# Performance work log

Measured on AMD Instinct MI355X. Metric: run time of the kernel, lower is better.

The kernel has to match this reference:

```python
import jax, jax.numpy as jnp
import numpy as np

NUM_HEADS = 16
HEAD_DIM = 80
DIM = NUM_HEADS * HEAD_DIM
SEQ = 2048
SCALE = HEAD_DIM ** -0.5


def rotate_half(x):
    x1, x2 = jnp.split(x, 2, axis=-1)
    return jnp.concatenate((-x2, x1), axis=-1)


def setup_inputs() -> dict:
    key = jax.random.key(0)
    ks = jax.random.split(key, 8)
    hidden_states = jax.random.normal(ks[0], (SEQ, DIM), dtype=jnp.float32)
    cu_seqlens = jnp.array([0, SEQ], dtype=jnp.int32)  # unused by the math
    # rotary embeddings for head_dim
    inv_freq = 1.0 / (10000.0 ** (jnp.arange(0, HEAD_DIM // 2, dtype=jnp.float32) / (HEAD_DIM // 2)))
    freqs = jnp.outer(jnp.arange(SEQ, dtype=jnp.float32), inv_freq)  # [S, hd/2]
    emb = jnp.concatenate((freqs, freqs), axis=-1)  # [S, hd]
    cos = jnp.cos(emb)
    sin = jnp.sin(emb)
    w_qkv = jax.random.normal(ks[1], (3 * DIM, DIM), dtype=jnp.float32) * (DIM ** -0.5)
    b_qkv = jax.random.normal(ks[2], (3 * DIM,), dtype=jnp.float32) * 0.02
    w_proj = jax.random.normal(ks[3], (DIM, DIM), dtype=jnp.float32) * (DIM ** -0.5)
    b_proj = jax.random.normal(ks[4], (DIM,), dtype=jnp.float32) * 0.02
    return {"hidden_states": hidden_states, "cu_seqlens": cu_seqlens, "cos": cos,
            "sin": sin, "w_qkv": w_qkv, "b_qkv": b_qkv, "w_proj": w_proj, "b_proj": b_proj}


def reference(hidden_states, cu_seqlens, cos, sin, w_qkv, b_qkv, w_proj, b_proj):
    S = hidden_states.shape[0]
    qkv = hidden_states @ w_qkv.T + b_qkv  # [S, 3*D]
    qkv = qkv.reshape(S, 3, NUM_HEADS, HEAD_DIM)
    q, k, v = qkv[:, 0], qkv[:, 1], qkv[:, 2]  # each [S, H, hd]
    c = cos[:, None, :]  # [S, 1, hd]
    s = sin[:, None, :]
    q = q * c + rotate_half(q) * s
    k = k * c + rotate_half(k) * s
    # SDPA, non-causal: [H, S, S]
    scores = jnp.einsum('shd,thd->hst', q, k) * SCALE
    attn = jax.nn.softmax(scores, axis=-1)
    out = jnp.einsum('hst,thd->shd', attn, v).reshape(S, DIM)
    return out @ w_proj.T + b_proj
```

## Files before the change

kernel.cpp:

```cpp
#include <hip/hip_runtime.h>


#define SEQLEN   2048
#define DIMM     1280
#define NHEADS   16
#define HD       80
#define QKV_N    3840
#define NSPLIT   4
#define KVSPAN   (SEQLEN / NSPLIT)
#define QSCALE_LOG2E 0.16130083587064776f

#define KSTRIDE  88
#define VFSTRIDE 24

#define EXP2F(x) __builtin_amdgcn_exp2f(x)

#define GLD16(gptr, lptr)                                                      \
    __builtin_amdgcn_global_load_lds(                                          \
        (const __attribute__((address_space(1))) void*)(gptr),                 \
        (__attribute__((address_space(3))) void*)(lptr), 16, 0, 0)

typedef float f32x4 __attribute__((ext_vector_type(4)));
typedef _Float16 half8 __attribute__((ext_vector_type(8)));
typedef _Float16 half4 __attribute__((ext_vector_type(4)));
typedef _Float16 half2v __attribute__((ext_vector_type(2)));

static __device__ __forceinline__ f32x4 mfma_16x16x32(half8 a, half8 b, f32x4 c) {
    return __builtin_amdgcn_mfma_f32_16x16x32_f16(a, b, c, 0, 0, 0);
}
static __device__ __forceinline__ f32x4 mfma_16x16x16(half4 a, half4 b, f32x4 c) {
    return __builtin_amdgcn_mfma_f32_16x16x16f16(a, b, c, 0, 0, 0);
}
static __device__ __forceinline__ half4 lo4(half8 v) {
    return __builtin_shufflevector(v, v, 0, 1, 2, 3);
}
static __device__ __forceinline__ half4 hi4(half8 v) {
    return __builtin_shufflevector(v, v, 4, 5, 6, 7);
}

__global__ __launch_bounds__(256)
void cast_all(const float* __restrict__ hs, const float* __restrict__ wq,
              const float* __restrict__ wp, _Float16* __restrict__ dhs,
              _Float16* __restrict__ dwq, _Float16* __restrict__ dwp) {
    const int n1 = SEQLEN * DIMM / 4, n2 = QKV_N * DIMM / 4, n3 = DIMM * DIMM / 4;
    int i = blockIdx.x * 256 + threadIdx.x;
    const float4* src; half4* dst; int j;
    if (i < n1)           { src = (const float4*)hs; dst = (half4*)dhs; j = i; }
    else if (i < n1 + n2) { src = (const float4*)wq; dst = (half4*)dwq; j = i - n1; }
    else if (i < n1 + n2 + n3) { src = (const float4*)wp; dst = (half4*)dwp; j = i - n1 - n2; }
    else return;
    const float4 v = src[j];
    half4 h;
    h.x = (_Float16)v.x; h.y = (_Float16)v.y;
    h.z = (_Float16)v.z; h.w = (_Float16)v.w;
    dst[j] = h;
}

template<bool OUT_F16>
__global__ __launch_bounds__(512, 4)
void gemm_bt128(const _Float16* __restrict__ A, const _Float16* __restrict__ B,
                const float* __restrict__ bias, void* __restrict__ Cout,
                int M, int N, int K) {
    __shared__ __align__(16) _Float16 As[2][128 * 32];
    __shared__ __align__(16) _Float16 Bs[2][128 * 32];
    const int tid  = threadIdx.x;
    const int lane = tid & 63;
    const int wave = tid >> 6;
    const int l15  = lane & 15;
    const int quad = lane >> 4;
    const int wm   = wave & 3;
    const int wn   = wave >> 2;
    const long bm = blockIdx.x, bn = blockIdx.y;

    const _Float16* Ag = A + bm * 128 * (long)K;
    const _Float16* Bg = B + bn * 128 * (long)K;

    const int srow = lane >> 2;
    const int scol = (lane & 3) * 8;
    f32x4 acc[2][4] = {};

    for (int k0 = 0; k0 < K; k0 += 64) {
        __syncthreads();
#pragma unroll
        for (int p = 0; p < 2; p++) {
            const int kp = k0 + p * 32;
            const long r = 16 * wave + srow;
            GLD16(Ag + r * K + kp + scol, &As[p][512 * wave + lane * 8]);
            GLD16(Bg + r * K + kp + scol, &Bs[p][512 * wave + lane * 8]);
        }
        __syncthreads();
#pragma unroll
        for (int p = 0; p < 2; p++) {
            half8 af[2], bf[4];
#pragma unroll
            for (int t = 0; t < 2; t++)
                af[t] = *(const half8*)&As[p][(wm * 32 + t * 16 + l15) * 32 + quad * 8];
#pragma unroll
            for (int t = 0; t < 4; t++)
                bf[t] = *(const half8*)&Bs[p][(wn * 64 + t * 16 + l15) * 32 + quad * 8];
#pragma unroll
            for (int mt = 0; mt < 2; mt++)
#pragma unroll
                for (int nt = 0; nt < 4; nt++)
                    acc[mt][nt] = mfma_16x16x32(af[mt], bf[nt], acc[mt][nt]);
        }
    }

    float bv[4];
#pragma unroll
    for (int nt = 0; nt < 4; nt++)
        bv[nt] = bias[bn * 128 + wn * 64 + nt * 16 + l15];

#pragma unroll
    for (int mt = 0; mt < 2; mt++) {
#pragma unroll
        for (int r = 0; r < 4; r++) {
            const long row = bm * 128 + wm * 32 + mt * 16 + quad * 4 + r;
#pragma unroll
            for (int nt = 0; nt < 4; nt++) {
                const long col = bn * 128 + wn * 64 + nt * 16 + l15;
                const float v = acc[mt][nt][r] + bv[nt];
                if (OUT_F16) ((_Float16*)Cout)[row * (long)N + col] = (_Float16)v;
                else         ((float*)Cout)[row * (long)N + col] = v;
            }
        }
    }
}

template<bool OUT_F16>
__global__ __launch_bounds__(256, 4)
void gemm_bt64(const _Float16* __restrict__ A, const _Float16* __restrict__ B,
               const float* __restrict__ bias, void* __restrict__ Cout,
               int M, int N, int K) {
    __shared__ __align__(16) _Float16 As[2][64 * 32];
    __shared__ __align__(16) _Float16 Bs[2][128 * 32];
    const int tid  = threadIdx.x;
    const int lane = tid & 63;
    const int wave = tid >> 6;
    const int l15  = lane & 15;
    const int quad = lane >> 4;
    const int wm   = wave & 1;
    const int wn   = wave >> 1;
    const long bm = blockIdx.x, bn = blockIdx.y;

    const _Float16* Ag = A + bm * 64 * (long)K;
    const _Float16* Bg = B + bn * 128 * (long)K;

    const int srow = lane >> 2;
    const int scol = (lane & 3) * 8;
    f32x4 acc[2][4] = {};

    for (int k0 = 0; k0 < K; k0 += 64) {
        __syncthreads();
#pragma unroll
        for (int p = 0; p < 2; p++) {
            const int kp = k0 + p * 32;
            const long arow = 16 * wave + srow;
            GLD16(Ag + arow * K + kp + scol, &As[p][512 * wave + lane * 8]);
#pragma unroll
            for (int cc = 0; cc < 2; cc++) {
                const int c = wave + cc * 4;
                const long brow = 16 * c + srow;
                GLD16(Bg + brow * K + kp + scol, &Bs[p][512 * c + lane * 8]);
            }
        }
        __syncthreads();
#pragma unroll
        for (int p = 0; p < 2; p++) {
            half8 af[2], bf[4];
#pragma unroll
            for (int t = 0; t < 2; t++)
                af[t] = *(const half8*)&As[p][(wm * 32 + t * 16 + l15) * 32 + quad * 8];
#pragma unroll
            for (int t = 0; t < 4; t++)
                bf[t] = *(const half8*)&Bs[p][(wn * 64 + t * 16 + l15) * 32 + quad * 8];
#pragma unroll
            for (int mt = 0; mt < 2; mt++)
#pragma unroll
                for (int nt = 0; nt < 4; nt++)
                    acc[mt][nt] = mfma_16x16x32(af[mt], bf[nt], acc[mt][nt]);
        }
    }

    float bv[4];
#pragma unroll
    for (int nt = 0; nt < 4; nt++)
        bv[nt] = bias[bn * 128 + wn * 64 + nt * 16 + l15];

#pragma unroll
    for (int mt = 0; mt < 2; mt++) {
#pragma unroll
        for (int r = 0; r < 4; r++) {
            const long row = bm * 64 + wm * 32 + mt * 16 + quad * 4 + r;
#pragma unroll
            for (int nt = 0; nt < 4; nt++) {
                const long col = bn * 128 + wn * 64 + nt * 16 + l15;
                const float v = acc[mt][nt][r] + bv[nt];
                if (OUT_F16) ((_Float16*)Cout)[row * (long)N + col] = (_Float16)v;
                else         ((float*)Cout)[row * (long)N + col] = v;
            }
        }
    }
}

__global__ __launch_bounds__(256)
void rope_repack_t(const _Float16* __restrict__ qkv,
                   const float* __restrict__ cosb,
                   const float* __restrict__ sinb,
                   _Float16* __restrict__ Qh,
                   _Float16* __restrict__ Kh,
                   _Float16* __restrict__ Vt) {
    const int s0 = blockIdx.x * 64;
    const int h  = blockIdx.y;
    __shared__ __align__(16) _Float16 Ts[64 * 88];
    const int tid = threadIdx.x;

    for (int i = tid; i < 640; i += 256) {
        const int r = i / 10, c = (i - r * 10) * 8;
        *(half8*)&Ts[r * 88 + c] =
            *(const half8*)&qkv[(long)(s0 + r) * QKV_N + 2 * DIMM + h * HD + c];
    }

    for (int i = tid; i < 320; i += 256) {
        const int r = i / 5, d = (i - r * 5) * 8;
        const _Float16* row = qkv + (long)(s0 + r) * QKV_N + h * HD;
        const half8 q0 = *(const half8*)&row[d];
        const half8 q1 = *(const half8*)&row[d + 40];
        const half8 k0 = *(const half8*)&row[DIMM + d];
        const half8 k1 = *(const half8*)&row[DIMM + d + 40];
        const float4 cA = *(const float4*)&cosb[(s0 + r) * HD + d];
        const float4 cB = *(const float4*)&cosb[(s0 + r) * HD + d + 4];
        const float4 sA = *(const float4*)&sinb[(s0 + r) * HD + d];
        const float4 sB = *(const float4*)&sinb[(s0 + r) * HD + d + 4];
        half8 qo0, qo1, ko0, ko1;
#pragma unroll
        for (int j = 0; j < 8; j++) {
            const float cj = (j < 4) ? cA[j] : cB[j - 4];
            const float sj = (j < 4) ? sA[j] : sB[j - 4];
            qo0[j] = (_Float16)(((float)q0[j] * cj - (float)q1[j] * sj) * QSCALE_LOG2E);
            qo1[j] = (_Float16)(((float)q1[j] * cj + (float)q0[j] * sj) * QSCALE_LOG2E);
            ko0[j] = (_Float16)((float)k0[j] * cj - (float)k1[j] * sj);
            ko1[j] = (_Float16)((float)k1[j] * cj + (float)k0[j] * sj);
        }
        const long o = ((long)h * SEQLEN + s0 + r) * HD;
        *(half8*)&Qh[o + d]      = qo0;
        *(half8*)&Qh[o + d + 40] = qo1;
        *(half8*)&Kh[o + d]      = ko0;
        *(half8*)&Kh[o + d + 40] = ko1;
    }
    __syncthreads();
    for (int i = tid; i < 640; i += 256) {
        const int d = i >> 3, sc = (i & 7) * 8;
        half8 v;
#pragma unroll
        for (int j = 0; j < 8; j++) v[j] = Ts[(sc + j) * 88 + d];
        *(half8*)&Vt[((long)h * HD + d) * SEQLEN + s0 + sc] = v;
    }
}

__global__ __launch_bounds__(512, 4)
void attn_kernel(const _Float16* __restrict__ Qh, const _Float16* __restrict__ Kh,
                 const _Float16* __restrict__ Vt,
                 _Float16* __restrict__ Ohat0, _Float16* __restrict__ Ohat1,
                 float* __restrict__ Lpart) {
    const int s0 = blockIdx.x * 256;
    const int h  = blockIdx.y;
    const int z  = blockIdx.z;
    __shared__ __align__(16) _Float16 Ks[64 * KSTRIDE];
    __shared__ __align__(16) _Float16 VF[5 * 64 * VFSTRIDE];

    const int tid  = threadIdx.x;
    const int lane = tid & 63;
    const int wave = tid >> 6;
    const int l15  = lane & 15;
    const int quad = lane >> 4;

    const int zBeg = z * KVSPAN, zEnd = zBeg + KVSPAN;

    const _Float16* Qg0 = Qh + ((long)h * SEQLEN + s0 + wave * 32 + l15) * HD;
    const _Float16* Qg1 = Qg0 + 16 * (long)HD;
    const half8 qA0 = *(const half8*)&Qg0[quad * 8];
    const half8 qA1 = *(const half8*)&Qg0[32 + quad * 8];
    const half4 qA2 = *(const half4*)&Qg0[64 + quad * 4];
    const half8 qB0 = *(const half8*)&Qg1[quad * 8];
    const half8 qB1 = *(const half8*)&Qg1[32 + quad * 8];
    const half4 qB2 = *(const half4*)&Qg1[64 + quad * 4];

    int offA, dsA, offB, dsB0, dsB1 = 0, offC = 0, dsC0 = 0, dsC1 = 0;
    {
        const int rA = tid / 10, cA = (tid - rA * 10) * 8;
        offA = rA * HD + cA;
        dsA  = rA * KSTRIDE + cA;
        if (tid < 128) {
            const int cB = tid + 512;
            const int rB = cB / 10, ccB = (cB - rB * 10) * 8;
            offB = rB * HD + ccB;
            dsB0 = rB * KSTRIDE + ccB;
        } else {
            const int v = tid - 128, d = v >> 3, c8 = (v & 7) * 8;
            offB = d * SEQLEN + c8;
            const int nt = d >> 4, ld = d & 15, ct = c8 >> 4, qb = (c8 & 15) >> 2;
            dsB0 = (nt * 64 + qb * 16 + ld) * VFSTRIDE + ct * 4;
            dsB1 = (nt * 64 + (qb + 1) * 16 + ld) * VFSTRIDE + ct * 4;
        }
        if (tid < 256) {
            const int v = tid + 384, d = v >> 3, c8 = (v & 7) * 8;
            offC = d * SEQLEN + c8;
            const int nt = d >> 4, ld = d & 15, ct = c8 >> 4, qb = (c8 & 15) >> 2;
            dsC0 = (nt * 64 + qb * 16 + ld) * VFSTRIDE + ct * 4;
            dsC1 = (nt * 64 + (qb + 1) * 16 + ld) * VFSTRIDE + ct * 4;
        }
    }
    const _Float16* KzBase = Kh + ((long)h * SEQLEN + zBeg) * HD;
    const _Float16* VzBase = Vt + (long)h * HD * SEQLEN + zBeg;

    half8 sga, sgb, sgc = (half8)(_Float16)0.f;
    sga = *(const half8*)(KzBase + offA);
    if (tid < 128) sgb = *(const half8*)(KzBase + offB);
    else           sgb = *(const half8*)(VzBase + offB);
    if (tid < 256) sgc = *(const half8*)(VzBase + offC);

    f32x4 oaccA[5] = {}, oaccB[5] = {};
    float laA0 = 0.f, laA1 = 0.f, laB0 = 0.f, laB1 = 0.f;
    const half2v ones2 = {(_Float16)1.f, (_Float16)1.f};

    for (int t0 = zBeg; t0 < zEnd; t0 += 64) {
        __syncthreads();
        *(half8*)&Ks[dsA] = sga;
        if (tid < 128) { *(half8*)&Ks[dsB0] = sgb; }
        else {
            *(half4*)&VF[dsB0] = lo4(sgb);
            *(half4*)&VF[dsB1] = hi4(sgb);
        }
        if (tid < 256) {
            *(half4*)&VF[dsC0] = lo4(sgc);
            *(half4*)&VF[dsC1] = hi4(sgc);
        }
        __syncthreads();

        if (t0 + 64 < zEnd) {
            const _Float16* KzT = KzBase + (long)(t0 + 64 - zBeg) * HD;
            const _Float16* VzT = VzBase + (t0 + 64 - zBeg);
            sga = *(const half8*)(KzT + offA);
            if (tid < 128) sgb = *(const half8*)(KzT + offB);
            else           sgb = *(const half8*)(VzT + offB);
            if (tid < 256) sgc = *(const half8*)(VzT + offC);
        }

        f32x4 saA[4] = {}, saB[4] = {};
        __builtin_amdgcn_s_setprio(1);
#pragma unroll
        for (int ct = 0; ct < 4; ct++) {
            const int kb = (ct * 16 + l15) * KSTRIDE;
            const half8 kf0 = *(const half8*)&Ks[kb + quad * 8];
            const half8 kf1 = *(const half8*)&Ks[kb + 32 + quad * 8];
            const half4 kf2 = *(const half4*)&Ks[kb + 64 + quad * 4];
            saA[ct] = mfma_16x16x32(kf0, qA0, saA[ct]);
            saB[ct] = mfma_16x16x32(kf0, qB0, saB[ct]);
            saA[ct] = mfma_16x16x32(kf1, qA1, saA[ct]);
            saB[ct] = mfma_16x16x32(kf1, qB1, saB[ct]);
            saA[ct] = mfma_16x16x16(kf2, qA2, saA[ct]);
            saB[ct] = mfma_16x16x16(kf2, qB2, saB[ct]);
        }
        __builtin_amdgcn_s_setprio(0);

        half4 pbA[4], pbB[4];
#pragma unroll
        for (int ct = 0; ct < 4; ct++) {
            {
                const float e0 = EXP2F(saA[ct][0]);
                const float e1 = EXP2F(saA[ct][1]);
                const float e2 = EXP2F(saA[ct][2]);
                const float e3 = EXP2F(saA[ct][3]);
                const half2v p01 = __builtin_bit_cast(half2v, __builtin_amdgcn_cvt_pkrtz(e0, e1));
                const half2v p23 = __builtin_bit_cast(half2v, __builtin_amdgcn_cvt_pkrtz(e2, e3));
                laA0 = __builtin_amdgcn_fdot2(p01, ones2, laA0, false);
                laA1 = __builtin_amdgcn_fdot2(p23, ones2, laA1, false);
                pbA[ct] = __builtin_shufflevector(p01, p23, 0, 1, 2, 3);
            }
            {
                const float e0 = EXP2F(saB[ct][0]);
                const float e1 = EXP2F(saB[ct][1]);
                const float e2 = EXP2F(saB[ct][2]);
                const float e3 = EXP2F(saB[ct][3]);
                const half2v p01 = __builtin_bit_cast(half2v, __builtin_amdgcn_cvt_pkrtz(e0, e1));
                const half2v p23 = __builtin_bit_cast(half2v, __builtin_amdgcn_cvt_pkrtz(e2, e3));
                laB0 = __builtin_amdgcn_fdot2(p01, ones2, laB0, false);
                laB1 = __builtin_amdgcn_fdot2(p23, ones2, laB1, false);
                pbB[ct] = __builtin_shufflevector(p01, p23, 0, 1, 2, 3);
            }
        }

        __builtin_amdgcn_s_setprio(1);
#pragma unroll
        for (int nt = 0; nt < 5; nt++) {
            const half8 va = *(const half8*)&VF[(nt * 64 + lane) * VFSTRIDE];
            const half8 vb = *(const half8*)&VF[(nt * 64 + lane) * VFSTRIDE + 8];
            oaccA[nt] = mfma_16x16x16(lo4(va), pbA[0], oaccA[nt]);
            oaccB[nt] = mfma_16x16x16(lo4(va), pbB[0], oaccB[nt]);
            oaccA[nt] = mfma_16x16x16(hi4(va), pbA[1], oaccA[nt]);
            oaccB[nt] = mfma_16x16x16(hi4(va), pbB[1], oaccB[nt]);
            oaccA[nt] = mfma_16x16x16(lo4(vb), pbA[2], oaccA[nt]);
            oaccB[nt] = mfma_16x16x16(lo4(vb), pbB[2], oaccB[nt]);
            oaccA[nt] = mfma_16x16x16(hi4(vb), pbA[3], oaccA[nt]);
            oaccB[nt] = mfma_16x16x16(hi4(vb), pbB[3], oaccB[nt]);
        }
        __builtin_amdgcn_s_setprio(0);
    }

    float lA = laA0 + laA1, lB = laB0 + laB1;
    lA += __shfl_xor(lA, 16); lA += __shfl_xor(lA, 32);
    lB += __shfl_xor(lB, 16); lB += __shfl_xor(lB, 32);
    const float invA = 1.0f / lA, invB = 1.0f / lB;

    _Float16* Oz = (z < 2) ? Ohat0 : Ohat1;
    const long obase = ((long)(z & 1) * NHEADS + h) * SEQLEN;
    const long lbase = ((long)z * NHEADS + h) * SEQLEN;
    const long rowA = s0 + wave * 32 + l15;
    const long rowB = rowA + 16;
#pragma unroll
    for (int nt = 0; nt < 5; nt++) {
        half4 oA, oB;
#pragma unroll
        for (int r = 0; r < 4; r++) {
            oA[r] = (_Float16)(oaccA[nt][r] * invA);
            oB[r] = (_Float16)(oaccB[nt][r] * invB);
        }
        *(half4*)&Oz[(obase + rowA) * HD + nt * 16 + quad * 4] = oA;
        *(half4*)&Oz[(obase + rowB) * HD + nt * 16 + quad * 4] = oB;
    }
    if (quad == 0) {
        Lpart[lbase + rowA] = lA;
        Lpart[lbase + rowB] = lB;
    }
}

__global__ __launch_bounds__(256)
void attn_combine(const _Float16* __restrict__ Ohat0,
                  const _Float16* __restrict__ Ohat1,
                  const float* __restrict__ Lp,
                  _Float16* __restrict__ attnb) {
    const int i = blockIdx.x * 256 + threadIdx.x;
    if (i >= SEQLEN * DIMM / 8) return;
    const int flat = i * 8;
    const int s = flat / DIMM;
    const int rem = flat - s * DIMM;
    const int h = rem / HD;
    const int d = rem - h * HD;
    float l[NSPLIT], lsum = 0.f;
#pragma unroll
    for (int zi = 0; zi < NSPLIT; zi++) {
        l[zi] = Lp[((long)zi * NHEADS + h) * SEQLEN + s];
        lsum += l[zi];
    }
    const float invl = 1.0f / lsum;
    float acc[8] = {};
#pragma unroll
    for (int zi = 0; zi < NSPLIT; zi++) {
        const _Float16* Oz = (zi < 2) ? Ohat0 : Ohat1;
        const long obase = ((long)(zi & 1) * NHEADS + h) * SEQLEN;
        const half8 o = *(const half8*)&Oz[(obase + s) * HD + d];
        const float w = l[zi] * invl;
#pragma unroll
        for (int j = 0; j < 8; j++) acc[j] += (float)o[j] * w;
    }
    half8 o;
#pragma unroll
    for (int j = 0; j < 8; j++) o[j] = (_Float16)acc[j];
    *(half8*)&attnb[(long)s * DIMM + rem] = o;
}

extern "C" void kernel_launch(void* const* d_in, const int* in_sizes, int n_in,
                              void* d_out, int out_size, void* d_ws, size_t ws_size,
                              hipStream_t stream) {
    const float* hs     = (const float*)d_in[0];
    const float* cosb   = (const float*)d_in[2];
    const float* sinb   = (const float*)d_in[3];
    const float* w_qkv  = (const float*)d_in[4];
    const float* b_qkv  = (const float*)d_in[5];
    const float* w_proj = (const float*)d_in[6];
    const float* b_proj = (const float*)d_in[7];
    float* out = (float*)d_out;

    _Float16* hsb    = (_Float16*)d_ws;
    _Float16* wqkvb  = hsb    + (long)SEQLEN * DIMM;
    _Float16* wprojb = wqkvb  + (long)QKV_N * DIMM;
    _Float16* qkv    = wprojb + (long)DIMM * DIMM;
    _Float16* Qh     = qkv    + (long)SEQLEN * QKV_N;
    _Float16* Kh     = Qh     + (long)NHEADS * SEQLEN * HD;
    _Float16* Vtb    = Kh     + (long)NHEADS * SEQLEN * HD;
    _Float16* attnb  = Vtb    + (long)NHEADS * HD * SEQLEN;

    _Float16* Ohat0  = (_Float16*)d_ws;
    float*    LpartB = (float*)(Ohat0 + (long)2 * NHEADS * SEQLEN * HD);
    _Float16* Ohat1  = qkv;

    {
        const int ntot = (SEQLEN * DIMM + QKV_N * DIMM + DIMM * DIMM) / 4;
        cast_all<<<(ntot + 255) / 256, 256, 0, stream>>>(
            hs, w_qkv, w_proj, hsb, wqkvb, wprojb);
    }

    gemm_bt128<true><<<dim3(SEQLEN / 128, QKV_N / 128), 512, 0, stream>>>(
        hsb, wqkvb, b_qkv, qkv, SEQLEN, QKV_N, DIMM);

    rope_repack_t<<<dim3(SEQLEN / 64, NHEADS), 256, 0, stream>>>(
        qkv, cosb, sinb, Qh, Kh, Vtb);

    attn_kernel<<<dim3(SEQLEN / 256, NHEADS, NSPLIT), 512, 0, stream>>>(
        Qh, Kh, Vtb, Ohat0, Ohat1, LpartB);

    attn_combine<<<(SEQLEN * DIMM / 8 + 255) / 256, 256, 0, stream>>>(
        Ohat0, Ohat1, LpartB, attnb);

    gemm_bt64<false><<<dim3(SEQLEN / 64, DIMM / 128), 256, 0, stream>>>(
        attnb, wprojb, b_proj, out, SEQLEN, DIMM, DIMM);
}
```

Measured before the change: 188.1 us.

## Double-buffer LDS tiles in both GEMM kernels to overlap loads with MFMA

Both GEMM kernels now keep two LDS buffers and issue async global-to-LDS loads for the next K-slice before running the MFMAs on the current slice, with one barrier per iteration instead of two. The aim is to hide global load latency behind matrix compute. LDS use per block doubles, and the bt64 launch bound drops to 3 blocks per SM, which may reduce occupancy. There is no explicit vmcnt wait before the barrier, so correctness relies on the compiler inserting waits for the LDS-direct loads.

```diff
diff --git a/kernel.cpp b/kernel.cpp
--- a/kernel.cpp
+++ b/kernel.cpp
@@ -61,8 +61,8 @@
 void gemm_bt128(const _Float16* __restrict__ A, const _Float16* __restrict__ B,
                 const float* __restrict__ bias, void* __restrict__ Cout,
                 int M, int N, int K) {
-    __shared__ __align__(16) _Float16 As[2][128 * 32];
-    __shared__ __align__(16) _Float16 Bs[2][128 * 32];
+    __shared__ __align__(16) _Float16 As[2][2][128 * 32];
+    __shared__ __align__(16) _Float16 Bs[2][2][128 * 32];
     const int tid  = threadIdx.x;
     const int lane = tid & 63;
     const int wave = tid >> 6;
@@ -77,33 +77,41 @@
 
     const int srow = lane >> 2;
     const int scol = (lane & 3) * 8;
+    const long r   = 16 * wave + srow;
     f32x4 acc[2][4] = {};
 
-    for (int k0 = 0; k0 < K; k0 += 64) {
-        __syncthreads();
+    auto stage = [&](int b, int k0) {
 #pragma unroll
         for (int p = 0; p < 2; p++) {
             const int kp = k0 + p * 32;
-            const long r = 16 * wave + srow;
-            GLD16(Ag + r * K + kp + scol, &As[p][512 * wave + lane * 8]);
-            GLD16(Bg + r * K + kp + scol, &Bs[p][512 * wave + lane * 8]);
-        }
-        __syncthreads();
+            GLD16(Ag + r * K + kp + scol, &As[b][p][512 * wave + lane * 8]);
+            GLD16(Bg + r * K + kp + scol, &Bs[b][p][512 * wave + lane * 8]);
+        }
+    };
+
+    stage(0, 0);
+    __syncthreads();
+
+    int cb = 0;
+    for (int k0 = 0; k0 < K; k0 += 64) {
+        if (k0 + 64 < K) stage(cb ^ 1, k0 + 64);
 #pragma unroll
         for (int p = 0; p < 2; p++) {
             half8 af[2], bf[4];
 #pragma unroll
             for (int t = 0; t < 2; t++)
-                af[t] = *(const half8*)&As[p][(wm * 32 + t * 16 + l15) * 32 + quad * 8];
+                af[t] = *(const half8*)&As[cb][p][(wm * 32 + t * 16 + l15) * 32 + quad * 8];
 #pragma unroll
             for (int t = 0; t < 4; t++)
-                bf[t] = *(const half8*)&Bs[p][(wn * 64 + t * 16 + l15) * 32 + quad * 8];
+                bf[t] = *(const half8*)&Bs[cb][p][(wn * 64 + t * 16 + l15) * 32 + quad * 8];
 #pragma unroll
             for (int mt = 0; mt < 2; mt++)
 #pragma unroll
                 for (int nt = 0; nt < 4; nt++)
                     acc[mt][nt] = mfma_16x16x32(af[mt], bf[nt], acc[mt][nt]);
         }
+        __syncthreads();
+        cb ^= 1;
     }
 
     float bv[4];
@@ -114,12 +122,12 @@
 #pragma unroll
     for (int mt = 0; mt < 2; mt++) {
 #pragma unroll
-        for (int r = 0; r < 4; r++) {
-            const long row = bm * 128 + wm * 32 + mt * 16 + quad * 4 + r;
+        for (int rr = 0; rr < 4; rr++) {
+            const long row = bm * 128 + wm * 32 + mt * 16 + quad * 4 + rr;
 #pragma unroll
             for (int nt = 0; nt < 4; nt++) {
                 const long col = bn * 128 + wn * 64 + nt * 16 + l15;
-                const float v = acc[mt][nt][r] + bv[nt];
+                const float v = acc[mt][nt][rr] + bv[nt];
                 if (OUT_F16) ((_Float16*)Cout)[row * (long)N + col] = (_Float16)v;
                 else         ((float*)Cout)[row * (long)N + col] = v;
             }
@@ -128,12 +136,12 @@
 }
 
 template<bool OUT_F16>
-__global__ __launch_bounds__(256, 4)
+__global__ __launch_bounds__(256, 3)
 void gemm_bt64(const _Float16* __restrict__ A, const _Float16* __restrict__ B,
                const float* __restrict__ bias, void* __restrict__ Cout,
                int M, int N, int K) {
-    __shared__ __align__(16) _Float16 As[2][64 * 32];
-    __shared__ __align__(16) _Float16 Bs[2][128 * 32];
+    __shared__ __align__(16) _Float16 As[2][2][64 * 32];
+    __shared__ __align__(16) _Float16 Bs[2][2][128 * 32];
     const int tid  = threadIdx.x;
     const int lane = tid & 63;
     const int wave = tid >> 6;
@@ -150,36 +158,44 @@
     const int scol = (lane & 3) * 8;
     f32x4 acc[2][4] = {};
 
-    for (int k0 = 0; k0 < K; k0 += 64) {
-        __syncthreads();
+    auto stage = [&](int b, int k0) {
 #pragma unroll
         for (int p = 0; p < 2; p++) {
             const int kp = k0 + p * 32;
             const long arow = 16 * wave + srow;
-            GLD16(Ag + arow * K + kp + scol, &As[p][512 * wave + lane * 8]);
+            GLD16(Ag + arow * K + kp + scol, &As[b][p][512 * wave + lane * 8]);
 #pragma unroll
             for (int cc = 0; cc < 2; cc++) {
                 const int c = wave + cc * 4;
                 const long brow = 16 * c + srow;
-                GLD16(Bg + brow * K + kp + scol, &Bs[p][512 * c + lane * 8]);
+                GLD16(Bg + brow * K + kp + scol, &Bs[b][p][512 * c + lane * 8]);
             }
         }
-        __syncthreads();
+    };
+
+    stage(0, 0);
+    __syncthreads();
+
+    int cb = 0;
+    for (int k0 = 0; k0 < K; k0 += 64) {
+        if (k0 + 64 < K) stage(cb ^ 1, k0 + 64);
 #pragma unroll
         for (int p = 0; p < 2; p++) {
             half8 af[2], bf[4];
 #pragma unroll
             for (int t = 0; t < 2; t++)
-                af[t] = *(const half8*)&As[p][(wm * 32 + t * 16 + l15) * 32 + quad * 8];
+                af[t] = *(const half8*)&As[cb][p][(wm * 32 + t * 16 + l15) * 32 + quad * 8];
 #pragma unroll
             for (int t = 0; t < 4; t++)
-                bf[t] = *(const half8*)&Bs[p][(wn * 64 + t * 16 + l15) * 32 + quad * 8];
+                bf[t] = *(const half8*)&Bs[cb][p][(wn * 64 + t * 16 + l15) * 32 + quad * 8];
 #pragma unroll
             for (int mt = 0; mt < 2; mt++)
 #pragma unroll
                 for (int nt = 0; nt < 4; nt++)
                     acc[mt][nt] = mfma_16x16x32(af[mt], bf[nt], acc[mt][nt]);
         }
+        __syncthreads();
+        cb ^= 1;
     }
 
     float bv[4];
@@ -190,12 +206,12 @@
 #pragma unroll
     for (int mt = 0; mt < 2; mt++) {
 #pragma unroll
-        for (int r = 0; r < 4; r++) {
-            const long row = bm * 64 + wm * 32 + mt * 16 + quad * 4 + r;
+        for (int rr = 0; rr < 4; rr++) {
+            const long row = bm * 64 + wm * 32 + mt * 16 + quad * 4 + rr;
 #pragma unroll
             for (int nt = 0; nt < 4; nt++) {
                 const long col = bn * 128 + wn * 64 + nt * 16 + l15;
-                const float v = acc[mt][nt][r] + bv[nt];
+                const float v = acc[mt][nt][rr] + bv[nt];
                 if (OUT_F16) ((_Float16*)Cout)[row * (long)N + col] = (_Float16)v;
                 else         ((float*)Cout)[row * (long)N + col] = v;
             }
```

Result: no change. 188.8 us (+0.4%).

## Stage 128-key K/V tiles per barrier pair and drop register prefetch

Applied to the files above, without the earlier changes.

The attention kernel now stages 128 keys of K and V into shared memory per iteration instead of 64, halving the number of barrier pairs per KV span. Each tile is processed as two 64-key halves with the same MFMA and exp code. The register-held prefetch of the next tile is removed, so global loads are issued at the top of each iteration and their latency is exposed before the store to LDS. Shared memory per block roughly doubles, which may lower occupancy. Separately, the gemm_bt64 launch bound is relaxed from 4 to 2 blocks per CU, giving the compiler more registers.

```diff
diff --git a/kernel.cpp b/kernel.cpp
--- a/kernel.cpp
+++ b/kernel.cpp
@@ -8,10 +8,12 @@
 #define QKV_N    3840
 #define NSPLIT   4
 #define KVSPAN   (SEQLEN / NSPLIT)
+#define KVBLK    128
 #define QSCALE_LOG2E 0.16130083587064776f
 
 #define KSTRIDE  88
 #define VFSTRIDE 24
+#define VHALF    (5 * 64 * VFSTRIDE)
 
 #define EXP2F(x) __builtin_amdgcn_exp2f(x)
 
@@ -128,7 +130,7 @@
 }
 
 template<bool OUT_F16>
-__global__ __launch_bounds__(256, 4)
+__global__ __launch_bounds__(256, 2)
 void gemm_bt64(const _Float16* __restrict__ A, const _Float16* __restrict__ B,
                const float* __restrict__ bias, void* __restrict__ Cout,
                int M, int N, int K) {
@@ -266,8 +268,8 @@
     const int s0 = blockIdx.x * 256;
     const int h  = blockIdx.y;
     const int z  = blockIdx.z;
-    __shared__ __align__(16) _Float16 Ks[64 * KSTRIDE];
-    __shared__ __align__(16) _Float16 VF[5 * 64 * VFSTRIDE];
+    __shared__ __align__(16) _Float16 Ks[KVBLK * KSTRIDE];
+    __shared__ __align__(16) _Float16 VF[2 * VHALF];
 
     const int tid  = threadIdx.x;
     const int lane = tid & 63;
@@ -286,126 +288,138 @@
     const half8 qB1 = *(const half8*)&Qg1[32 + quad * 8];
     const half4 qB2 = *(const half4*)&Qg1[64 + quad * 4];
 
-    int offA, dsA, offB, dsB0, dsB1 = 0, offC = 0, dsC0 = 0, dsC1 = 0;
+    int offA, dsA, offB, dsB, offC, dsC0, dsC1 = 0;
+    int offD, dsD0, dsD1, offE, dsE0, dsE1;
     {
         const int rA = tid / 10, cA = (tid - rA * 10) * 8;
-        offA = rA * HD + cA;
-        dsA  = rA * KSTRIDE + cA;
-        if (tid < 128) {
-            const int cB = tid + 512;
-            const int rB = cB / 10, ccB = (cB - rB * 10) * 8;
-            offB = rB * HD + ccB;
-            dsB0 = rB * KSTRIDE + ccB;
+        offA = rA * HD + cA;  dsA = rA * KSTRIDE + cA;
+        const int iB = tid + 512;
+        const int rB = iB / 10, cB = (iB - rB * 10) * 8;
+        offB = rB * HD + cB;  dsB = rB * KSTRIDE + cB;
+        if (tid < 256) {
+            const int iC = tid + 1024;
+            const int rC = iC / 10, cC = (iC - rC * 10) * 8;
+            offC = rC * HD + cC;  dsC0 = rC * KSTRIDE + cC;
         } else {
-            const int v = tid - 128, d = v >> 3, c8 = (v & 7) * 8;
-            offB = d * SEQLEN + c8;
-            const int nt = d >> 4, ld = d & 15, ct = c8 >> 4, qb = (c8 & 15) >> 2;
-            dsB0 = (nt * 64 + qb * 16 + ld) * VFSTRIDE + ct * 4;
-            dsB1 = (nt * 64 + (qb + 1) * 16 + ld) * VFSTRIDE + ct * 4;
-        }
-        if (tid < 256) {
-            const int v = tid + 384, d = v >> 3, c8 = (v & 7) * 8;
+            const int vi = tid - 256, d = vi >> 4, c8 = (vi & 15) * 8;
             offC = d * SEQLEN + c8;
-            const int nt = d >> 4, ld = d & 15, ct = c8 >> 4, qb = (c8 & 15) >> 2;
-            dsC0 = (nt * 64 + qb * 16 + ld) * VFSTRIDE + ct * 4;
-            dsC1 = (nt * 64 + (qb + 1) * 16 + ld) * VFSTRIDE + ct * 4;
+            const int hf = c8 >> 6, c8l = c8 & 63;
+            const int nt = d >> 4, ld = d & 15, ct = c8l >> 4, qb = (c8l & 15) >> 2;
+            dsC0 = hf * VHALF + (nt * 64 + qb * 16 + ld) * VFSTRIDE + ct * 4;
+            dsC1 = hf * VHALF + (nt * 64 + (qb + 1) * 16 + ld) * VFSTRIDE + ct * 4;
+        }
+        {
+            const int vi = tid + 256, d = vi >> 4, c8 = (vi & 15) * 8;
+            offD = d * SEQLEN + c8;
+            const int hf = c8 >> 6, c8l = c8 & 63;
+            const int nt = d >> 4, ld = d & 15, ct = c8l >> 4, qb = (c8l & 15) >> 2;
+            dsD0 = hf * VHALF + (nt * 64 + qb * 16 + ld) * VFSTRIDE + ct * 4;
+            dsD1 = hf * VHALF + (nt * 64 + (qb + 1) * 16 + ld) * VFSTRIDE + ct * 4;
+        }
+        {
+            const int vi = tid + 768, d = vi >> 4, c8 = (vi & 15) * 8;
+            offE = d * SEQLEN + c8;
+            const int hf = c8 >> 6, c8l = c8 & 63;
+            const int nt = d >> 4, ld = d & 15, ct = c8l >> 4, qb = (c8l & 15) >> 2;
+            dsE0 = hf * VHALF + (nt * 64 + qb * 16 + ld) * VFSTRIDE + ct * 4;
+            dsE1 = hf * VHALF + (nt * 64 + (qb + 1) * 16 + ld) * VFSTRIDE + ct * 4;
         }
     }
     const _Float16* KzBase = Kh + ((long)h * SEQLEN + zBeg) * HD;
     const _Float16* VzBase = Vt + (long)h * HD * SEQLEN + zBeg;
-
-    half8 sga, sgb, sgc = (half8)(_Float16)0.f;
-    sga = *(const half8*)(KzBase + offA);
-    if (tid < 128) sgb = *(const half8*)(KzBase + offB);
-    else           sgb = *(const half8*)(VzBase + offB);
-    if (tid < 256) sgc = *(const half8*)(VzBase + offC);
 
     f32x4 oaccA[5] = {}, oaccB[5] = {};
     float laA0 = 0.f, laA1 = 0.f, laB0 = 0.f, laB1 = 0.f;
     const half2v ones2 = {(_Float16)1.f, (_Float16)1.f};
 
-    for (int t0 = zBeg; t0 < zEnd; t0 += 64) {
+    for (int t0 = zBeg; t0 < zEnd; t0 += KVBLK) {
+        const _Float16* KzT = KzBase + (long)(t0 - zBeg) * HD;
+        const _Float16* VzT = VzBase + (t0 - zBeg);
+        const half8 sga = *(const half8*)(KzT + offA);
+        const half8 sgb = *(const half8*)(KzT + offB);
+        half8 sgc;
+        if (tid < 256) sgc = *(const half8*)(KzT + offC);
+        else           sgc = *(const half8*)(VzT + offC);
+        const half8 sgd = *(const half8*)(VzT + offD);
+        const half8 sge = *(const half8*)(VzT + offE);
+
         __syncthreads();
         *(half8*)&Ks[dsA] = sga;
-        if (tid < 128) { *(half8*)&Ks[dsB0] = sgb; }
+        *(half8*)&Ks[dsB] = sgb;
+        if (tid < 256) { *(half8*)&Ks[dsC0] = sgc; }
         else {
-            *(half4*)&VF[dsB0] = lo4(sgb);
-            *(half4*)&VF[dsB1] = hi4(sgb);
-        }
-        if (tid < 256) {
             *(half4*)&VF[dsC0] = lo4(sgc);
             *(half4*)&VF[dsC1] = hi4(sgc);
         }
+        *(half4*)&VF[dsD0] = lo4(sgd);
+        *(half4*)&VF[dsD1] = hi4(sgd);
+        *(half4*)&VF[dsE0] = lo4(sge);
+        *(half4*)&VF[dsE1] = hi4(sge);
         __syncthreads();
 
-        if (t0 + 64 < zEnd) {
-            const _Float16* KzT = KzBase + (long)(t0 + 64 - zBeg) * HD;
-            const _Float16* VzT = VzBase + (t0 + 64 - zBeg);
-            sga = *(const half8*)(KzT + offA);
-            if (tid < 128) sgb = *(const half8*)(KzT + offB);
-            else           sgb = *(const half8*)(VzT + offB);
-            if (tid < 256) sgc = *(const half8*)(VzT + offC);
-        }
-
-        f32x4 saA[4] = {}, saB[4] = {};
-        __builtin_amdgcn_s_setprio(1);
-#pragma unroll
-        for (int ct = 0; ct < 4; ct++) {
-            const int kb = (ct * 16 + l15) * KSTRIDE;
-            const half8 kf0 = *(const half8*)&Ks[kb + quad * 8];
-            const half8 kf1 = *(const half8*)&Ks[kb + 32 + quad * 8];
-            const half4 kf2 = *(const half4*)&Ks[kb + 64 + quad * 4];
-            saA[ct] = mfma_16x16x32(kf0, qA0, saA[ct]);
-            saB[ct] = mfma_16x16x32(kf0, qB0, saB[ct]);
-            saA[ct] = mfma_16x16x32(kf1, qA1, saA[ct]);
-            saB[ct] = mfma_16x16x32(kf1, qB1, saB[ct]);
-            saA[ct] = mfma_16x16x16(kf2, qA2, saA[ct]);
-            saB[ct] = mfma_16x16x16(kf2, qB2, saB[ct]);
-        }
-        __builtin_amdgcn_s_setprio(0);
-
-        half4 pbA[4], pbB[4];
-#pragma unroll
-        for (int ct = 0; ct < 4; ct++) {
-            {
-                const float e0 = EXP2F(saA[ct][0]);
-                const float e1 = EXP2F(saA[ct][1]);
-                const float e2 = EXP2F(saA[ct][2]);
-                const float e3 = EXP2F(saA[ct][3]);
-                const half2v p01 = __builtin_bit_cast(half2v, __builtin_amdgcn_cvt_pkrtz(e0, e1));
-                const half2v p23 = __builtin_bit_cast(half2v, __builtin_amdgcn_cvt_pkrtz(e2, e3));
-                laA0 = __builtin_amdgcn_fdot2(p01, ones2, laA0, false);
-                laA1 = __builtin_amdgcn_fdot2(p23, ones2, laA1, false);
-                pbA[ct] = __builtin_shufflevector(p01, p23, 0, 1, 2, 3);
+#pragma unroll
+        for (int hf = 0; hf < 2; hf++) {
+            f32x4 saA[4] = {}, saB[4] = {};
+            __builtin_amdgcn_s_setprio(1);
+#pragma unroll
+            for (int ct = 0; ct < 4; ct++) {
+                const int kb = (hf * 64 + ct * 16 + l15) * KSTRIDE;
+                const half8 kf0 = *(const half8*)&Ks[kb + quad * 8];
+                const half8 kf1 = *(const half8*)&Ks[kb + 32 + quad * 8];
+                const half4 kf2 = *(const half4*)&Ks[kb + 64 + quad * 4];
+                saA[ct] = mfma_16x16x32(kf0, qA0, saA[ct]);
+                saB[ct] = mfma_16x16x32(kf0, qB0, saB[ct]);
+                saA[ct] = mfma_16x16x32(kf1, qA1, saA[ct]);
+                saB[ct] = mfma_16x16x32(kf1, qB1, saB[ct]);
+                saA[ct] = mfma_16x16x16(kf2, qA2, saA[ct]);
+                saB[ct] = mfma_16x16x16(kf2, qB2, saB[ct]);
             }
-            {
-                const float e0 = EXP2F(saB[ct][0]);
-                const float e1 = EXP2F(saB[ct][1]);
-                const float e2 = EXP2F(saB[ct][2]);
-                const float e3 = EXP2F(saB[ct][3]);
-                const half2v p01 = __builtin_bit_cast(half2v, __builtin_amdgcn_cvt_pkrtz(e0, e1));
-                const half2v p23 = __builtin_bit_cast(half2v, __builtin_amdgcn_cvt_pkrtz(e2, e3));
-                laB0 = __builtin_amdgcn_fdot2(p01, ones2, laB0, false);
-                laB1 = __builtin_amdgcn_fdot2(p23, ones2, laB1, false);
-                pbB[ct] = __builtin_shufflevector(p01, p23, 0, 1, 2, 3);
+            __builtin_amdgcn_s_setprio(0);
+
+            half4 pbA[4], pbB[4];
+#pragma unroll
+            for (int ct = 0; ct < 4; ct++) {
+                {
+                    const float e0 = EXP2F(saA[ct][0]);
+                    const float e1 = EXP2F(saA[ct][1]);
+                    const float e2 = EXP2F(saA[ct][2]);
+                    const float e3 = EXP2F(saA[ct][3]);
+                    const half2v p01 = __builtin_bit_cast(half2v, __builtin_amdgcn_cvt_pkrtz(e0, e1));
+                    const half2v p23 = __builtin_bit_cast(half2v, __builtin_amdgcn_cvt_pkrtz(e2, e3));
+                    laA0 = __builtin_amdgcn_fdot2(p01, ones2, laA0, false);
+                    laA1 = __builtin_amdgcn_fdot2(p23, ones2, laA1, false);
+                    pbA[ct] = __builtin_shufflevector(p01, p23, 0, 1, 2, 3);
+                }
+                {
+                    const float e0 = EXP2F(saB[ct][0]);
+                    const float e1 = EXP2F(saB[ct][1]);
+                    const float e2 = EXP2F(saB[ct][2]);
+                    const float e3 = EXP2F(saB[ct][3]);
+                    const half2v p01 = __builtin_bit_cast(half2v, __builtin_amdgcn_cvt_pkrtz(e0, e1));
+                    const half2v p23 = __builtin_bit_cast(half2v, __builtin_amdgcn_cvt_pkrtz(e2, e3));
+                    laB0 = __builtin_amdgcn_fdot2(p01, ones2, laB0, false);
+                    laB1 = __builtin_amdgcn_fdot2(p23, ones2, laB1, false);
+                    pbB[ct] = __builtin_shufflevector(p01, p23, 0, 1, 2, 3);
+                }
             }
-        }
-
-        __builtin_amdgcn_s_setprio(1);
-#pragma unroll
-        for (int nt = 0; nt < 5; nt++) {
-            const half8 va = *(const half8*)&VF[(nt * 64 + lane) * VFSTRIDE];
-            const half8 vb = *(const half8*)&VF[(nt * 64 + lane) * VFSTRIDE + 8];
-            oaccA[nt] = mfma_16x16x16(lo4(va), pbA[0], oaccA[nt]);
-            oaccB[nt] = mfma_16x16x16(lo4(va), pbB[0], oaccB[nt]);
-            oaccA[nt] = mfma_16x16x16(hi4(va), pbA[1], oaccA[nt]);
-            oaccB[nt] = mfma_16x16x16(hi4(va), pbB[1], oaccB[nt]);
-            oaccA[nt] = mfma_16x16x16(lo4(vb), pbA[2], oaccA[nt]);
-            oaccB[nt] = mfma_16x16x16(lo4(vb), pbB[2], oaccB[nt]);
-            oaccA[nt] = mfma_16x16x16(hi4(vb), pbA[3], oaccA[nt]);
-            oaccB[nt] = mfma_16x16x16(hi4(vb), pbB[3], oaccB[nt]);
-        }
-        __builtin_amdgcn_s_setprio(0);
+
+            __builtin_amdgcn_s_setprio(1);
+#pragma unroll
+            for (int nt = 0; nt < 5; nt++) {
+                const int vb0 = hf * VHALF + (nt * 64 + lane) * VFSTRIDE;
+                const half8 va = *(const half8*)&VF[vb0];
+                const half8 vb = *(const half8*)&VF[vb0 + 8];
+                oaccA[nt] = mfma_16x16x16(lo4(va), pbA[0], oaccA[nt]);
+                oaccB[nt] = mfma_16x16x16(lo4(va), pbB[0], oaccB[nt]);
+                oaccA[nt] = mfma_16x16x16(hi4(va), pbA[1], oaccA[nt]);
+                oaccB[nt] = mfma_16x16x16(hi4(va), pbB[1], oaccB[nt]);
+                oaccA[nt] = mfma_16x16x16(lo4(vb), pbA[2], oaccA[nt]);
+                oaccB[nt] = mfma_16x16x16(lo4(vb), pbB[2], oaccB[nt]);
+                oaccA[nt] = mfma_16x16x16(hi4(vb), pbA[3], oaccA[nt]);
+                oaccB[nt] = mfma_16x16x16(hi4(vb), pbB[3], oaccB[nt]);
+            }
+            __builtin_amdgcn_s_setprio(0);
+        }
     }
 
     float lA = laA0 + laA1, lB = laB0 + laB1;
```

Result: no change. 186.8 us (-0.7%).
